# Kernel optimization log

Hardware: AMD Instinct MI355X
Metric: run time of the kernel (lower is better)

Reference implementation:

```python
import jax, jax.numpy as jnp
import numpy as np

DIM = 768

def setup_inputs() -> dict:
    key = jax.random.key(0)
    k1, k2, k3, k4 = jax.random.split(key, 4)
    B, N, C = 32, 577, DIM
    x = jax.random.normal(k1, (B, N, C), dtype=jnp.float32)
    # torch Linear weights: (out_features, in_features)
    w_qkv = jax.random.normal(k2, (3 * C, C), dtype=jnp.float32) * (C ** -0.5)
    w_proj = jax.random.normal(k3, (C, C), dtype=jnp.float32) * (C ** -0.5)
    b_proj = jax.random.normal(k4, (C,), dtype=jnp.float32) * 0.02
    return {"x": x, "w_qkv": w_qkv, "w_proj": w_proj, "b_proj": b_proj}

def reference(x, w_qkv, w_proj, b_proj):
    B, N, C = x.shape
    attn_size = int((N - 1) ** 0.5)
    scale = C ** -0.5
    qkv = (x @ w_qkv.T).reshape(B, N, 3, C)          # [B,N,3,C]
    qkv = jnp.transpose(qkv, (2, 0, 1, 3))           # [3,B,N,C]
    q, k, v = qkv[0], qkv[1], qkv[2]
    attn = jax.nn.softmax(jnp.einsum('bnc,bmc->bnm', q, k) * scale, axis=-1)  # [B,N,N]
    y = jnp.einsum('bnm,bmc->bnc', attn, v)          # [B,N,C]
    # faithful to original: transpose(1,2) then reshape back (data permutation)
    y = jnp.transpose(y, (0, 2, 1)).reshape(B, N, C)
    out = y @ w_proj.T + b_proj
    token_attn = attn[:, 0, 1:].reshape(B, 1, attn_size, attn_size)
    return (out, token_attn)
```

## Files before the change

### kernel.cpp

```cpp
#include <hip/hip_runtime.h>


typedef __attribute__((ext_vector_type(4))) float f32x4;
typedef __attribute__((ext_vector_type(8))) short short8;
typedef __attribute__((ext_vector_type(8))) unsigned short ushort8v;
typedef __attribute__((ext_vector_type(4))) unsigned short ushort4v;

#define TILE 128
#define BK 64

#define NB 32
#define SEQ 577
#define SEQP 640
#define DIM 768
#define MTOT (NB * SEQ)
#define VTLD (NB * SEQP)
#define KC 0.05205949529797614f

__device__ __forceinline__ unsigned short f2bf(float f) {
  union { float f; unsigned u; } x; x.f = f;
  unsigned r = x.u + 0x7fffu + ((x.u >> 16) & 1u);
  return (unsigned short)(r >> 16);
}

__device__ __forceinline__ void gload16(const unsigned short* g, unsigned short* l) {
  __builtin_amdgcn_global_load_lds(
      (const __attribute__((address_space(1))) unsigned int*)g,
      (__attribute__((address_space(3))) unsigned int*)l, 16, 0, 0);
}

__device__ __forceinline__ int swiz(int lin, int nblk) {
  int xcd = lin & 7, pos = lin >> 3;
  int per = nblk >> 3, rem = nblk & 7;
  return xcd * per + (xcd < rem ? xcd : rem) + pos;
}

__device__ __forceinline__ void gemm_core(
    unsigned short* smem,
    const unsigned short* __restrict__ A, int ldA, int rowmaxA, int blkM,
    const unsigned short* __restrict__ B, int ldB, int rowmaxB, int blkN,
    int K, f32x4 acc[4][4])
{
  unsigned short* sA = smem;
  unsigned short* sB = smem + TILE * BK;
  const int t = threadIdx.x;
  const int lane = t & 63;
  const int wave = t >> 6;
  const int wr = (wave >> 1) * 64;
  const int wc = (wave & 1) * 64;
  const int lrow = lane & 15;
  const int quad = lane >> 4;

  for (int k0 = 0; k0 < K; k0 += BK) {
#pragma unroll
    for (int it = 0; it < 4; ++it) {
      int tt = t + it * 256;
      int rr = tt >> 3;
      int gc = (tt & 7) ^ (rr & 7);
      int ra = blkM + rr; if (ra > rowmaxA) ra = rowmaxA;
      int rb = blkN + rr; if (rb > rowmaxB) rb = rowmaxB;
      gload16(A + (size_t)ra * ldA + k0 + gc * 8, sA + tt * 8);
      gload16(B + (size_t)rb * ldB + k0 + gc * 8, sB + tt * 8);
    }
    __syncthreads();
#pragma unroll
    for (int kk = 0; kk < 2; ++kk) {
      short8 af[4], bfr[4];
#pragma unroll
      for (int i = 0; i < 4; ++i) {
        int m = wr + i * 16 + lrow;
        af[i] = *(const short8*)(sA + m * BK + (((kk * 4 + quad) ^ (m & 7)) * 8));
      }
#pragma unroll
      for (int j = 0; j < 4; ++j) {
        int n = wc + j * 16 + lrow;
        bfr[j] = *(const short8*)(sB + n * BK + (((kk * 4 + quad) ^ (n & 7)) * 8));
      }
#pragma unroll
      for (int i = 0; i < 4; ++i)
#pragma unroll
        for (int j = 0; j < 4; ++j)
          acc[i][j] = __builtin_amdgcn_mfma_f32_16x16x32_bf16(af[i], bfr[j], acc[i][j], 0, 0, 0);
    }
    __syncthreads();
  }
}

#define N4X  3545088
#define N4W1 442368
#define N4W2 147456
__global__ __launch_bounds__(256) void k_cvt3(
    const float* __restrict__ x, const float* __restrict__ w1, const float* __restrict__ w2,
    unsigned short* __restrict__ xo, unsigned short* __restrict__ w1o,
    unsigned short* __restrict__ w2o) {
  int i = blockIdx.x * 256 + threadIdx.x;
  const float4* src; ushort4* dst; int off;
  if (i < N4X)                 { src = (const float4*)x;  dst = (ushort4*)xo;  off = i; }
  else if (i < N4X + N4W1)     { src = (const float4*)w1; dst = (ushort4*)w1o; off = i - N4X; }
  else                         { src = (const float4*)w2; dst = (ushort4*)w2o; off = i - N4X - N4W1; }
  float4 v = src[off];
  ushort4 o;
  o.x = f2bf(v.x); o.y = f2bf(v.y); o.z = f2bf(v.z); o.w = f2bf(v.w);
  dst[off] = o;
}

__global__ __launch_bounds__(256, 2) void k_qkv(
    const unsigned short* __restrict__ xb, const unsigned short* __restrict__ wb,
    unsigned short* __restrict__ qb, unsigned short* __restrict__ kb,
    unsigned short* __restrict__ vt) {
  __shared__ unsigned short smem[2 * TILE * BK];
  f32x4 acc[4][4];
#pragma unroll
  for (int i = 0; i < 4; ++i)
#pragma unroll
    for (int j = 0; j < 4; ++j) acc[i][j] = (f32x4){0.f, 0.f, 0.f, 0.f};

  int lin = swiz(blockIdx.y * 18 + blockIdx.x, 18 * 160);
  const int tN = lin % 18;
  const int tMall = lin / 18;
  const int b = tMall / 5;
  const int mt = tMall % 5;
  const unsigned short* A = xb + (size_t)b * SEQ * DIM;
  gemm_core(smem, A, DIM, SEQ - 1, mt * TILE, wb, DIM, 3 * DIM - 1, tN * TILE, DIM, acc);

  const int t = threadIdx.x, lane = t & 63, wave = t >> 6;
  const int wr = (wave >> 1) * 64, wc = (wave & 1) * 64;
  const int l15 = lane & 15, quad = lane >> 4;
  const int sel = tN / 6, cbase = (tN % 6) * TILE;

  if (sel < 2) {
#pragma unroll
    for (int i = 0; i < 4; ++i)
#pragma unroll
      for (int j = 0; j < 4; ++j)
#pragma unroll
        for (int r = 0; r < 4; ++r) {
          int m = wr + i * 16 + quad * 4 + r, n = wc + j * 16 + l15;
          smem[m * TILE + (n ^ ((m & 7) << 3))] = f2bf(acc[i][j][r]);
        }
  } else {
#pragma unroll
    for (int i = 0; i < 4; ++i)
#pragma unroll
      for (int j = 0; j < 4; ++j)
#pragma unroll
        for (int r = 0; r < 4; ++r) {
          int m = wr + i * 16 + quad * 4 + r, n = wc + j * 16 + l15;
          smem[n * TILE + (m ^ ((n & 7) << 3))] = f2bf(acc[i][j][r]);
        }
  }
  __syncthreads();

  if (sel < 2) {
    unsigned short* dst = sel == 0 ? qb : kb;
#pragma unroll
    for (int s = 0; s < 8; ++s) {
      int idx = t + s * 256, rr = idx >> 4, seg = idx & 15;
      int nn = mt * TILE + rr;
      if (nn < SEQ) {
        ushort8v v = *(const ushort8v*)(smem + rr * TILE + ((seg * 8) ^ ((rr & 7) << 3)));
        *(ushort8v*)(dst + ((size_t)(b * SEQ + nn)) * DIM + cbase + seg * 8) = v;
      }
    }
  } else {
#pragma unroll
    for (int s = 0; s < 8; ++s) {
      int idx = t + s * 256, rr = idx >> 4, seg = idx & 15;
      int c = cbase + rr;
      int nn0 = mt * TILE + seg * 8;
      if (nn0 < SEQ) {
        ushort8v v = *(const ushort8v*)(smem + rr * TILE + ((seg * 8) ^ ((rr & 7) << 3)));
        unsigned short* dp = vt + (size_t)c * VTLD + (size_t)b * SEQP + nn0;
        if (nn0 + 8 <= SEQ) *(ushort8v*)dp = v;
        else {
#pragma unroll
          for (int e = 0; e < 8; ++e) if (nn0 + e < SEQ) dp[e] = v[e];
        }
      }
    }
  }
}

__global__ __launch_bounds__(256, 2) void k_logits(
    const unsigned short* __restrict__ qb, const unsigned short* __restrict__ kb,
    unsigned short* __restrict__ Pt, float* __restrict__ part) {
  __shared__ unsigned short smem[2 * TILE * BK];
  __shared__ float rpart[128][2];
  f32x4 acc[4][4];
#pragma unroll
  for (int i = 0; i < 4; ++i)
#pragma unroll
    for (int j = 0; j < 4; ++j) acc[i][j] = (f32x4){0.f, 0.f, 0.f, 0.f};
  int lin = swiz(blockIdx.y * 25 + blockIdx.x, 25 * NB);
  const int b = lin / 25;
  const int tM = (lin % 25) / 5, tN = lin % 5;
  const unsigned short* A = qb + (size_t)b * SEQ * DIM;
  const unsigned short* B = kb + (size_t)b * SEQ * DIM;
  gemm_core(smem, A, DIM, SEQ - 1, tM * TILE, B, DIM, SEQ - 1, tN * TILE, DIM, acc);

  const int t = threadIdx.x, lane = t & 63, wave = t >> 6;
  const int wr = (wave >> 1) * 64, wc = (wave & 1) * 64;
  const int l15 = lane & 15, quad = lane >> 4;

#pragma unroll
  for (int i = 0; i < 4; ++i)
#pragma unroll
    for (int j = 0; j < 4; ++j) {
      int ng = tN * TILE + wc + j * 16 + l15;
#pragma unroll
      for (int r = 0; r < 4; ++r) {
        float e = exp2f(acc[i][j][r] * KC);
        acc[i][j][r] = (ng < SEQ) ? e : 0.f;
      }
    }
#pragma unroll
  for (int i = 0; i < 4; ++i)
#pragma unroll
    for (int r = 0; r < 4; ++r) {
      float p = acc[i][0][r] + acc[i][1][r] + acc[i][2][r] + acc[i][3][r];
      p += __shfl_xor(p, 1); p += __shfl_xor(p, 2);
      p += __shfl_xor(p, 4); p += __shfl_xor(p, 8);
      if (l15 == 0) rpart[wr + i * 16 + quad * 4 + r][wave & 1] = p;
    }
  __syncthreads();
  if (t < 128) {
    int row = tM * TILE + t;
    part[((size_t)b * 5 + tN) * SEQP + row] = rpart[t][0] + rpart[t][1];
  }
#pragma unroll
  for (int i = 0; i < 4; ++i)
#pragma unroll
    for (int j = 0; j < 4; ++j)
#pragma unroll
      for (int r = 0; r < 4; ++r) {
        int m = wr + i * 16 + quad * 4 + r, n = wc + j * 16 + l15;
        smem[m * TILE + (n ^ ((m & 7) << 3))] = f2bf(acc[i][j][r]);
      }
  __syncthreads();
  unsigned short* Pb = Pt + (size_t)b * SEQP * SEQP;
#pragma unroll
  for (int s = 0; s < 8; ++s) {
    int idx = t + s * 256, rr = idx >> 4, seg = idx & 15;
    int m = tM * TILE + rr;
    ushort8v v = *(const ushort8v*)(smem + rr * TILE + ((seg * 8) ^ ((rr & 7) << 3)));
    *(ushort8v*)(Pb + (size_t)m * SEQP + tN * TILE + seg * 8) = v;
  }
}

__global__ __launch_bounds__(256) void k_tok(const unsigned short* __restrict__ Pt,
                                             const float* __restrict__ part,
                                             float* __restrict__ tok) {
  const int b = blockIdx.x, t = threadIdx.x;
  const float* pp = part + (size_t)b * 5 * SEQP;
  float inv = 1.0f / (pp[0] + pp[SEQP] + pp[2 * SEQP] + pp[3 * SEQP] + pp[4 * SEQP]);
  const unsigned short* Pr = Pt + (size_t)b * SEQP * SEQP;
  for (int n = t; n < SEQ; n += 256) {
    if (n >= 1) {
      union { unsigned u; float f; } c; c.u = ((unsigned)Pr[n]) << 16;
      tok[(size_t)b * (SEQ - 1) + n - 1] = c.f * inv;
    }
  }
}

__global__ __launch_bounds__(256, 2) void k_pv(
    const unsigned short* __restrict__ Pt, const unsigned short* __restrict__ vt,
    const float* __restrict__ part, unsigned short* __restrict__ yf) {
  __shared__ unsigned short smem[2 * TILE * BK];
  __shared__ float linv[128];
  f32x4 acc[4][4];
#pragma unroll
  for (int i = 0; i < 4; ++i)
#pragma unroll
    for (int j = 0; j < 4; ++j) acc[i][j] = (f32x4){0.f, 0.f, 0.f, 0.f};
  int lin = swiz(blockIdx.y * 30 + blockIdx.x, 30 * NB);
  const int b = lin / 30;
  const int tM = (lin % 30) / 6, tN = lin % 6;
  const unsigned short* A = Pt + (size_t)b * SEQP * SEQP;
  gemm_core(smem, A, SEQP, SEQP - 1, tM * TILE,
            vt + (size_t)b * SEQP, VTLD, DIM - 1, tN * TILE, SEQP, acc);

  const int t = threadIdx.x, lane = t & 63, wave = t >> 6;
  const int wr = (wave >> 1) * 64, wc = (wave & 1) * 64;
  const int l15 = lane & 15, quad = lane >> 4;

  if (t < 128) {
    int row = tM * TILE + t;
    const float* pp = part + (size_t)b * 5 * SEQP + row;
    float s = pp[0] + pp[SEQP] + pp[2 * SEQP] + pp[3 * SEQP] + pp[4 * SEQP];
    linv[t] = 1.0f / s;
  }
  __syncthreads();

#pragma unroll
  for (int i = 0; i < 4; ++i)
#pragma unroll
    for (int j = 0; j < 4; ++j)
#pragma unroll
      for (int r = 0; r < 4; ++r) {
        int m = wr + i * 16 + quad * 4 + r, n = wc + j * 16 + l15;
        smem[n * TILE + (m ^ ((n & 7) << 3))] = f2bf(acc[i][j][r] * linv[m]);
      }
  __syncthreads();

  const int rowc = t >> 1, h = t & 1;
  const int c = tN * TILE + rowc;
  const int sw = (rowc & 7) << 3;
  unsigned short* yrow = yf + (size_t)b * DIM * SEQ + (size_t)c * SEQ;
  int m0 = tM * TILE + h * 64;
  int mend = m0 + 64; if (mend > SEQ) mend = SEQ;
  int m = m0;
  while (m < mend && ((c + m) & 3)) { yrow[m] = smem[rowc * TILE + ((m - tM * TILE) ^ sw)]; ++m; }
  for (; m + 4 <= mend; m += 4) {
    ushort4v v;
#pragma unroll
    for (int e = 0; e < 4; ++e) v[e] = smem[rowc * TILE + ((m + e - tM * TILE) ^ sw)];
    *(ushort4v*)(yrow + m) = v;
  }
  for (; m < mend; ++m) yrow[m] = smem[rowc * TILE + ((m - tM * TILE) ^ sw)];
}

__global__ __launch_bounds__(256, 2) void k_proj(
    const unsigned short* __restrict__ yf, const unsigned short* __restrict__ wpb,
    const float* __restrict__ bproj, float* __restrict__ out) {
  __shared__ unsigned short smem[2 * TILE * BK];
  f32x4 acc[4][4];
#pragma unroll
  for (int i = 0; i < 4; ++i)
#pragma unroll
    for (int j = 0; j < 4; ++j) acc[i][j] = (f32x4){0.f, 0.f, 0.f, 0.f};
  int lin = swiz(blockIdx.y * 6 + blockIdx.x, 6 * 145);
  const int tM = lin / 6, tN = lin % 6;
  gemm_core(smem, yf, DIM, MTOT - 1, tM * TILE, wpb, DIM, DIM - 1, tN * TILE, DIM, acc);

  const int lane = threadIdx.x & 63, wave = threadIdx.x >> 6;
#pragma unroll
  for (int i = 0; i < 4; ++i)
#pragma unroll
    for (int j = 0; j < 4; ++j) {
      int n = tN * TILE + (wave & 1) * 64 + j * 16 + (lane & 15);
      float bias = bproj[n];
#pragma unroll
      for (int r = 0; r < 4; ++r) {
        int m = tM * TILE + (wave >> 1) * 64 + i * 16 + (lane >> 4) * 4 + r;
        if (m < MTOT) out[(size_t)m * DIM + n] = acc[i][j][r] + bias;
      }
    }
}

extern "C" void kernel_launch(void* const* d_in, const int* in_sizes, int n_in,
                              void* d_out, int out_size, void* d_ws, size_t ws_size,
                              hipStream_t stream) {
  const float* x     = (const float*)d_in[0];
  const float* wqkv  = (const float*)d_in[1];
  const float* wproj = (const float*)d_in[2];
  const float* bproj = (const float*)d_in[3];
  float* out = (float*)d_out;
  float* tok = out + (size_t)NB * SEQ * DIM;

  char* ws = (char*)d_ws;
  unsigned short* xb    = (unsigned short*)(ws + 0);
  unsigned short* wqkvb = (unsigned short*)(ws + 28360704);
  unsigned short* wprojb= (unsigned short*)(ws + 31899648);
  unsigned short* qb    = (unsigned short*)(ws + 33079296);
  unsigned short* kb    = (unsigned short*)(ws + 61440000);
  unsigned short* vt    = (unsigned short*)(ws + 89800704);
  unsigned short* Pt    = (unsigned short*)(ws + 121257984);
  float*          part  = (float*)         (ws + 147472384);
  unsigned short* yf    = (unsigned short*)(ws + 147881984);

  k_cvt3<<<16152, 256, 0, stream>>>(x, wqkv, wproj, xb, wqkvb, wprojb);
  k_qkv<<<dim3(18, 160), 256, 0, stream>>>(xb, wqkvb, qb, kb, vt);
  k_logits<<<dim3(25, NB), 256, 0, stream>>>(qb, kb, Pt, part);
  k_tok<<<NB, 256, 0, stream>>>(Pt, part, tok);
  k_pv<<<dim3(30, NB), 256, 0, stream>>>(Pt, vt, part, yf);
  k_proj<<<dim3(6, 145), 256, 0, stream>>>(yf, wprojb, bproj, out);
}
```

Baseline: 307.6 us.

## Swap GEMM operand roles for transposed outputs, fuse token kernel, coalesce proj stores

The V-part of the QKV GEMM and the PV GEMM now swap A/B operands, so the accumulator already holds the transposed tile. This drops the strided transposed LDS writes in the epilogue. The separate token-attention kernel is folded into k_pv, which removes one launch. The projection epilogue now stages fp32 results through LDS in two halves and writes coalesced float4 rows instead of scattered scalar stores, at the cost of extra barriers.

```diff
diff --git a/kernel.cpp b/kernel.cpp
--- a/kernel.cpp
+++ b/kernel.cpp
@@ -21,6 +21,10 @@
   union { float f; unsigned u; } x; x.f = f;
   unsigned r = x.u + 0x7fffu + ((x.u >> 16) & 1u);
   return (unsigned short)(r >> 16);
+}
+
+__device__ __forceinline__ float bf2f(unsigned short v) {
+  union { unsigned u; float f; } x; x.u = ((unsigned)v) << 16; return x.f;
 }
 
 __device__ __forceinline__ void gload16(const unsigned short* g, unsigned short* l) {
@@ -120,15 +124,15 @@
   const int tMall = lin / 18;
   const int b = tMall / 5;
   const int mt = tMall % 5;
-  const unsigned short* A = xb + (size_t)b * SEQ * DIM;
-  gemm_core(smem, A, DIM, SEQ - 1, mt * TILE, wb, DIM, 3 * DIM - 1, tN * TILE, DIM, acc);
+  const int sel = tN / 6, cbase = (tN % 6) * TILE;
+  const unsigned short* Xb = xb + (size_t)b * SEQ * DIM;
 
   const int t = threadIdx.x, lane = t & 63, wave = t >> 6;
   const int wr = (wave >> 1) * 64, wc = (wave & 1) * 64;
   const int l15 = lane & 15, quad = lane >> 4;
-  const int sel = tN / 6, cbase = (tN % 6) * TILE;
 
   if (sel < 2) {
+    gemm_core(smem, Xb, DIM, SEQ - 1, mt * TILE, wb, DIM, 3 * DIM - 1, tN * TILE, DIM, acc);
 #pragma unroll
     for (int i = 0; i < 4; ++i)
 #pragma unroll
@@ -138,20 +142,7 @@
           int m = wr + i * 16 + quad * 4 + r, n = wc + j * 16 + l15;
           smem[m * TILE + (n ^ ((m & 7) << 3))] = f2bf(acc[i][j][r]);
         }
-  } else {
-#pragma unroll
-    for (int i = 0; i < 4; ++i)
-#pragma unroll
-      for (int j = 0; j < 4; ++j)
-#pragma unroll
-        for (int r = 0; r < 4; ++r) {
-          int m = wr + i * 16 + quad * 4 + r, n = wc + j * 16 + l15;
-          smem[n * TILE + (m ^ ((n & 7) << 3))] = f2bf(acc[i][j][r]);
-        }
-  }
-  __syncthreads();
-
-  if (sel < 2) {
+    __syncthreads();
     unsigned short* dst = sel == 0 ? qb : kb;
 #pragma unroll
     for (int s = 0; s < 8; ++s) {
@@ -163,18 +154,29 @@
       }
     }
   } else {
+    gemm_core(smem, wb, DIM, 3 * DIM - 1, 2 * DIM + cbase, Xb, DIM, SEQ - 1, mt * TILE, DIM, acc);
+#pragma unroll
+    for (int i = 0; i < 4; ++i)
+#pragma unroll
+      for (int j = 0; j < 4; ++j)
+#pragma unroll
+        for (int r = 0; r < 4; ++r) {
+          int m = wr + i * 16 + quad * 4 + r, n = wc + j * 16 + l15;
+          smem[m * TILE + (n ^ ((m & 7) << 3))] = f2bf(acc[i][j][r]);
+        }
+    __syncthreads();
 #pragma unroll
     for (int s = 0; s < 8; ++s) {
       int idx = t + s * 256, rr = idx >> 4, seg = idx & 15;
       int c = cbase + rr;
-      int nn0 = mt * TILE + seg * 8;
-      if (nn0 < SEQ) {
+      int n0 = mt * TILE + seg * 8;
+      if (n0 < SEQ) {
         ushort8v v = *(const ushort8v*)(smem + rr * TILE + ((seg * 8) ^ ((rr & 7) << 3)));
-        unsigned short* dp = vt + (size_t)c * VTLD + (size_t)b * SEQP + nn0;
-        if (nn0 + 8 <= SEQ) *(ushort8v*)dp = v;
+        unsigned short* dp = vt + (size_t)c * VTLD + (size_t)b * SEQP + n0;
+        if (n0 + 8 <= SEQ) *(ushort8v*)dp = v;
         else {
 #pragma unroll
-          for (int e = 0; e < 8; ++e) if (nn0 + e < SEQ) dp[e] = v[e];
+          for (int e = 0; e < 8; ++e) if (n0 + e < SEQ) dp[e] = v[e];
         }
       }
     }
@@ -247,24 +249,10 @@
   }
 }
 
-__global__ __launch_bounds__(256) void k_tok(const unsigned short* __restrict__ Pt,
-                                             const float* __restrict__ part,
-                                             float* __restrict__ tok) {
-  const int b = blockIdx.x, t = threadIdx.x;
-  const float* pp = part + (size_t)b * 5 * SEQP;
-  float inv = 1.0f / (pp[0] + pp[SEQP] + pp[2 * SEQP] + pp[3 * SEQP] + pp[4 * SEQP]);
-  const unsigned short* Pr = Pt + (size_t)b * SEQP * SEQP;
-  for (int n = t; n < SEQ; n += 256) {
-    if (n >= 1) {
-      union { unsigned u; float f; } c; c.u = ((unsigned)Pr[n]) << 16;
-      tok[(size_t)b * (SEQ - 1) + n - 1] = c.f * inv;
-    }
-  }
-}
-
 __global__ __launch_bounds__(256, 2) void k_pv(
     const unsigned short* __restrict__ Pt, const unsigned short* __restrict__ vt,
-    const float* __restrict__ part, unsigned short* __restrict__ yf) {
+    const float* __restrict__ part, unsigned short* __restrict__ yf,
+    float* __restrict__ tok) {
   __shared__ unsigned short smem[2 * TILE * BK];
   __shared__ float linv[128];
   f32x4 acc[4][4];
@@ -274,17 +262,16 @@
     for (int j = 0; j < 4; ++j) acc[i][j] = (f32x4){0.f, 0.f, 0.f, 0.f};
   int lin = swiz(blockIdx.y * 30 + blockIdx.x, 30 * NB);
   const int b = lin / 30;
-  const int tM = (lin % 30) / 6, tN = lin % 6;
-  const unsigned short* A = Pt + (size_t)b * SEQP * SEQP;
-  gemm_core(smem, A, SEQP, SEQP - 1, tM * TILE,
-            vt + (size_t)b * SEQP, VTLD, DIM - 1, tN * TILE, SEQP, acc);
+  const int tC = (lin % 30) / 5, tT = lin % 5;
+  gemm_core(smem, vt + (size_t)b * SEQP, VTLD, DIM - 1, tC * TILE,
+            Pt + (size_t)b * SEQP * SEQP, SEQP, SEQP - 1, tT * TILE, SEQP, acc);
 
   const int t = threadIdx.x, lane = t & 63, wave = t >> 6;
   const int wr = (wave >> 1) * 64, wc = (wave & 1) * 64;
   const int l15 = lane & 15, quad = lane >> 4;
 
   if (t < 128) {
-    int row = tM * TILE + t;
+    int row = tT * TILE + t;
     const float* pp = part + (size_t)b * 5 * SEQP + row;
     float s = pp[0] + pp[SEQP] + pp[2 * SEQP] + pp[3 * SEQP] + pp[4 * SEQP];
     linv[t] = 1.0f / s;
@@ -292,31 +279,42 @@
   __syncthreads();
 
 #pragma unroll
-  for (int i = 0; i < 4; ++i)
-#pragma unroll
-    for (int j = 0; j < 4; ++j)
+  for (int j = 0; j < 4; ++j) {
+    float ln = linv[wc + j * 16 + l15];
+#pragma unroll
+    for (int i = 0; i < 4; ++i)
 #pragma unroll
       for (int r = 0; r < 4; ++r) {
         int m = wr + i * 16 + quad * 4 + r, n = wc + j * 16 + l15;
-        smem[n * TILE + (m ^ ((n & 7) << 3))] = f2bf(acc[i][j][r] * linv[m]);
-      }
+        smem[m * TILE + (n ^ ((m & 7) << 3))] = f2bf(acc[i][j][r] * ln);
+      }
+  }
   __syncthreads();
 
   const int rowc = t >> 1, h = t & 1;
-  const int c = tN * TILE + rowc;
+  const int c = tC * TILE + rowc;
   const int sw = (rowc & 7) << 3;
-  unsigned short* yrow = yf + (size_t)b * DIM * SEQ + (size_t)c * SEQ;
-  int m0 = tM * TILE + h * 64;
-  int mend = m0 + 64; if (mend > SEQ) mend = SEQ;
-  int m = m0;
-  while (m < mend && ((c + m) & 3)) { yrow[m] = smem[rowc * TILE + ((m - tM * TILE) ^ sw)]; ++m; }
-  for (; m + 4 <= mend; m += 4) {
+  unsigned short* yrow = yf + ((size_t)b * DIM + c) * SEQ;
+  int n0 = tT * TILE + h * 64;
+  int nend = n0 + 64; if (nend > SEQ) nend = SEQ;
+  int n = n0;
+  while (n < nend && ((c + n) & 3)) { yrow[n] = smem[rowc * TILE + ((n - tT * TILE) ^ sw)]; ++n; }
+  for (; n + 4 <= nend; n += 4) {
     ushort4v v;
 #pragma unroll
-    for (int e = 0; e < 4; ++e) v[e] = smem[rowc * TILE + ((m + e - tM * TILE) ^ sw)];
-    *(ushort4v*)(yrow + m) = v;
-  }
-  for (; m < mend; ++m) yrow[m] = smem[rowc * TILE + ((m - tM * TILE) ^ sw)];
+    for (int e = 0; e < 4; ++e) v[e] = smem[rowc * TILE + ((n + e - tT * TILE) ^ sw)];
+    *(ushort4v*)(yrow + n) = v;
+  }
+  for (; n < nend; ++n) yrow[n] = smem[rowc * TILE + ((n - tT * TILE) ^ sw)];
+
+  if (tC == 0 && t < 128) {
+    const float* pp = part + (size_t)b * 5 * SEQP;
+    float inv0 = 1.0f / (pp[0] + pp[SEQP] + pp[2 * SEQP] + pp[3 * SEQP] + pp[4 * SEQP]);
+    int nt = tT * TILE + t;
+    if (nt >= 1 && nt < SEQ)
+      tok[(size_t)b * (SEQ - 1) + nt - 1] =
+          bf2f(Pt[(size_t)b * SEQP * SEQP + nt]) * inv0;
+  }
 }
 
 __global__ __launch_bounds__(256, 2) void k_proj(
@@ -332,19 +330,38 @@
   const int tM = lin / 6, tN = lin % 6;
   gemm_core(smem, yf, DIM, MTOT - 1, tM * TILE, wpb, DIM, DIM - 1, tN * TILE, DIM, acc);
 
-  const int lane = threadIdx.x & 63, wave = threadIdx.x >> 6;
-#pragma unroll
-  for (int i = 0; i < 4; ++i)
-#pragma unroll
-    for (int j = 0; j < 4; ++j) {
-      int n = tN * TILE + (wave & 1) * 64 + j * 16 + (lane & 15);
-      float bias = bproj[n];
-#pragma unroll
-      for (int r = 0; r < 4; ++r) {
-        int m = tM * TILE + (wave >> 1) * 64 + i * 16 + (lane >> 4) * 4 + r;
-        if (m < MTOT) out[(size_t)m * DIM + n] = acc[i][j][r] + bias;
-      }
-    }
+  const int t = threadIdx.x, lane = t & 63, wave = t >> 6;
+  const int wc = (wave & 1) * 64;
+  const int l15 = lane & 15, quad = lane >> 4;
+  float* smem32 = (float*)smem;
+  const int wquad = wave >> 1;
+
+#pragma unroll
+  for (int p = 0; p < 2; ++p) {
+    if (wquad == p) {
+#pragma unroll
+      for (int j = 0; j < 4; ++j) {
+        int n = wc + j * 16 + l15;
+        float bias = bproj[tN * TILE + n];
+#pragma unroll
+        for (int i = 0; i < 4; ++i)
+#pragma unroll
+          for (int r = 0; r < 4; ++r)
+            smem32[(i * 16 + quad * 4 + r) * TILE + n] = acc[i][j][r] + bias;
+      }
+    }
+    __syncthreads();
+#pragma unroll
+    for (int s = 0; s < 8; ++s) {
+      int idx = t + s * 256;
+      int rloc = idx >> 5, col4 = idx & 31;
+      int m = tM * TILE + p * 64 + rloc;
+      if (m < MTOT)
+        ((float4*)(out + (size_t)m * DIM + tN * TILE))[col4] =
+            ((const float4*)(smem32 + rloc * TILE))[col4];
+    }
+    __syncthreads();
+  }
 }
 
 extern "C" void kernel_launch(void* const* d_in, const int* in_sizes, int n_in,
@@ -371,7 +388,6 @@
   k_cvt3<<<16152, 256, 0, stream>>>(x, wqkv, wproj, xb, wqkvb, wprojb);
   k_qkv<<<dim3(18, 160), 256, 0, stream>>>(xb, wqkvb, qb, kb, vt);
   k_logits<<<dim3(25, NB), 256, 0, stream>>>(qb, kb, Pt, part);
-  k_tok<<<NB, 256, 0, stream>>>(Pt, part, tok);
-  k_pv<<<dim3(30, NB), 256, 0, stream>>>(Pt, vt, part, yf);
+  k_pv<<<dim3(30, NB), 256, 0, stream>>>(Pt, vt, part, yf, tok);
   k_proj<<<dim3(6, 145), 256, 0, stream>>>(yf, wprojb, bproj, out);
 }
```

Result: faster. 298.4 us (-3.0%).
